# Performance work log

Measured on AMD Instinct MI355X. Metric: run time of the kernel, lower is better.

The kernel has to match this reference:

```python
import jax, jax.numpy as jnp
import numpy as np

B, T, DIM = 1, 2048, 4096
N_HEADS, N_KV_HEADS, HEAD_DIM = 32, 8, 128
N_REP = N_HEADS // N_KV_HEADS
ROPE_THETA = 10000.0


def setup_inputs() -> dict:
    key = jax.random.key(0)
    ks = jax.random.split(key, 6)
    # rotary angle tables: [T, head_dim//2]
    inv_freq = 1.0 / (ROPE_THETA ** (np.arange(0, HEAD_DIM, 2, dtype=np.float32) / HEAD_DIM))
    angles = np.arange(T, dtype=np.float32)[:, None] * inv_freq[None, :]
    scale = 0.02
    return {
        "x": jax.random.normal(ks[0], (B, T, DIM), dtype=jnp.float32),
        "rope_cos": jnp.asarray(np.cos(angles)),
        "rope_sin": jnp.asarray(np.sin(angles)),
        "wq": jax.random.normal(ks[1], (DIM, N_HEADS * HEAD_DIM), dtype=jnp.float32) * scale,
        "wk": jax.random.normal(ks[2], (DIM, N_KV_HEADS * HEAD_DIM), dtype=jnp.float32) * scale,
        "wv": jax.random.normal(ks[3], (DIM, N_KV_HEADS * HEAD_DIM), dtype=jnp.float32) * scale,
        "wo": jax.random.normal(ks[4], (N_HEADS * HEAD_DIM, DIM), dtype=jnp.float32) * scale,
    }


def _apply_rope(x, cos, sin):
    # x: [B, T, H, D]; cos/sin: [T, D//2] -- complex multiply on (even, odd) pairs
    xr = x.astype(jnp.float32).reshape(*x.shape[:-1], -1, 2)
    a, b = xr[..., 0], xr[..., 1]
    c = cos[None, : x.shape[1], None, :]
    s = sin[None, : x.shape[1], None, :]
    rot = jnp.stack([a * c - b * s, a * s + b * c], axis=-1)
    return rot.reshape(x.shape).astype(x.dtype)


def reference(x, rope_cos, rope_sin, wq, wk, wv, wo):
    Bq, Tq, _ = x.shape
    q = (x @ wq).reshape(Bq, Tq, N_HEADS, HEAD_DIM)
    k = (x @ wk).reshape(Bq, Tq, N_KV_HEADS, HEAD_DIM)
    v = (x @ wv).reshape(Bq, Tq, N_KV_HEADS, HEAD_DIM)
    q = _apply_rope(q, rope_cos, rope_sin)
    k = _apply_rope(k, rope_cos, rope_sin)
    # GQA: group query heads with their shared KV head instead of materializing repeated K/V
    qg = q.reshape(Bq, Tq, N_KV_HEADS, N_REP, HEAD_DIM)
    scale = 1.0 / jnp.sqrt(jnp.asarray(HEAD_DIM, dtype=q.dtype))
    scores = jnp.einsum("bqgrd,bkgd->bgrqk", qg, k) * scale  # [B,G,R,T,T]
    causal = jnp.tril(jnp.ones((Tq, Tq), dtype=bool))
    scores = jnp.where(causal[None, None, None], scores, jnp.finfo(scores.dtype).min)
    attn = jax.nn.softmax(scores, axis=-1)
    ctx = jnp.einsum("bgrqk,bkgd->bqgrd", attn, v).reshape(Bq, Tq, N_HEADS * HEAD_DIM)
    return ctx @ wo
```

## Files before the change

kernel.cpp:

```cpp
#include <hip/hip_runtime.h>
#include <hip/hip_bf16.h>

#define T_SEQ 2048
#define DIM 4096
#define NH 32
#define NKV 8
#define HD 128
#define QKV_N 6144

typedef __bf16 bf16x8 __attribute__((ext_vector_type(8)));
typedef float f32x4 __attribute__((ext_vector_type(4)));

__device__ __forceinline__ void storev(float* p, float v) { *p = v; }
__device__ __forceinline__ void storev(__hip_bfloat16* p, float v) { *p = __float2bfloat16(v); }

__device__ __forceinline__ float bf2f(unsigned short u) {
    unsigned int t = ((unsigned int)u) << 16;
    return __builtin_bit_cast(float, t);
}

__device__ __forceinline__ void gl_lds16(const __hip_bfloat16* g, __hip_bfloat16* l) {
    __builtin_amdgcn_global_load_lds(
        (const __attribute__((address_space(1))) unsigned int*)g,
        (__attribute__((address_space(3))) unsigned int*)l, 16, 0, 0);
}

__global__ void cast_x(const float* __restrict__ in, __hip_bfloat16* __restrict__ out, int n) {
    int i = (blockIdx.x * 256 + threadIdx.x) * 4;
    if (i < n) {
        float4 v = *(const float4*)(in + i);
        out[i + 0] = __float2bfloat16(v.x);
        out[i + 1] = __float2bfloat16(v.y);
        out[i + 2] = __float2bfloat16(v.z);
        out[i + 3] = __float2bfloat16(v.w);
    }
}

__global__ void tcast(const float* __restrict__ in, __hip_bfloat16* __restrict__ out,
                      int R, int C, int out_stride, int row_off) {
    __shared__ float tile[64][65];
    int tid = threadIdx.x;
    int r0 = blockIdx.y * 64, c0 = blockIdx.x * 64;
    for (int it = 0; it < 4; it++) {
        int row = (tid >> 4) + 16 * it;
        int c4 = (tid & 15) * 4;
        float4 v = *(const float4*)&in[(size_t)(r0 + row) * C + c0 + c4];
        tile[row][c4 + 0] = v.x;
        tile[row][c4 + 1] = v.y;
        tile[row][c4 + 2] = v.z;
        tile[row][c4 + 3] = v.w;
    }
    __syncthreads();
    for (int it = 0; it < 2; it++) {
        int orow = (tid >> 3) + 32 * it;
        int oc8 = (tid & 7) * 8;
        __hip_bfloat16 tmp[8];
        for (int j = 0; j < 8; j++)
            tmp[j] = __float2bfloat16(tile[oc8 + j][orow]);
        *(uint4*)&out[(size_t)(c0 + orow + row_off) * out_stride + r0 + oc8] = *(uint4*)tmp;
    }
}

__global__ void vtrans(const __hip_bfloat16* __restrict__ qkv, __hip_bfloat16* __restrict__ vt) {
    __shared__ __hip_bfloat16 tile[32][33];
    int tx = threadIdx.x, ty = threadIdx.y;
    int t0 = blockIdx.x * 32, d0 = blockIdx.y * 32, g = blockIdx.z;
    for (int k = 0; k < 4; k++)
        tile[ty + 8 * k][tx] = qkv[(size_t)(t0 + ty + 8 * k) * QKV_N + 5120 + g * HD + d0 + tx];
    __syncthreads();
    for (int k = 0; k < 4; k++)
        vt[(size_t)g * HD * T_SEQ + (size_t)(d0 + ty + 8 * k) * T_SEQ + t0 + tx] =
            tile[tx][ty + 8 * k];
}

__global__ void rope_kernel(__hip_bfloat16* qkv, const float* __restrict__ cosb,
                            const float* __restrict__ sinb) {
    int idx = blockIdx.x * 256 + threadIdx.x;
    int t = idx / 640;
    int col = (idx % 640) * 8;
    int i0 = (col & 127) >> 1;
    float f = col < DIM ? 0.08838834764831845f : 1.0f;
    size_t base = (size_t)t * QKV_N + col;
    unsigned short u[8];
    *(uint4*)u = *(const uint4*)&qkv[base];
    float4 cv = *(const float4*)&cosb[t * 64 + i0];
    float4 sv = *(const float4*)&sinb[t * 64 + i0];
    float c[4] = {cv.x, cv.y, cv.z, cv.w}, s[4] = {sv.x, sv.y, sv.z, sv.w};
    __hip_bfloat16 o[8];
    for (int j = 0; j < 4; j++) {
        float a = bf2f(u[2 * j]), b = bf2f(u[2 * j + 1]);
        o[2 * j]     = __float2bfloat16((a * c[j] - b * s[j]) * f);
        o[2 * j + 1] = __float2bfloat16((a * s[j] + b * c[j]) * f);
    }
    *(uint4*)&qkv[base] = *(uint4*)o;
}

template <typename OutT>
__global__ __launch_bounds__(256, 2) void gemm_bt(const __hip_bfloat16* __restrict__ A,
                                                  const __hip_bfloat16* __restrict__ Bt,
                                                  OutT* __restrict__ C, int M, int N, int K) {
    __shared__ __hip_bfloat16 sA[2][128 * 32];
    __shared__ __hip_bfloat16 sB[2][128 * 32];
    int tid = threadIdx.x;
    int wave = tid >> 6, lane = tid & 63, quad = lane >> 4, l15 = lane & 15;
    int wm = wave >> 1, wn = wave & 1;
    int m0 = blockIdx.y * 128, n0 = blockIdx.x * 128;
    f32x4 acc[4][4] = {};
    for (int k0 = 0; k0 < K; k0 += 64) {
        __syncthreads();
        for (int r = 0; r < 2; r++) {
            int seg = tid + 256 * r;
            int row = seg >> 2, col = (seg & 3) * 8;
            gl_lds16(&A[(size_t)(m0 + row) * K + k0 + col],       &sA[0][row * 32 + col]);
            gl_lds16(&A[(size_t)(m0 + row) * K + k0 + 32 + col],  &sA[1][row * 32 + col]);
            gl_lds16(&Bt[(size_t)(n0 + row) * K + k0 + col],      &sB[0][row * 32 + col]);
            gl_lds16(&Bt[(size_t)(n0 + row) * K + k0 + 32 + col], &sB[1][row * 32 + col]);
        }
        __syncthreads();
        for (int ks = 0; ks < 2; ks++) {
            bf16x8 af[4], bfr[4];
            for (int i = 0; i < 4; i++)
                af[i] = *(const bf16x8*)&sA[ks][(wm * 64 + i * 16 + l15) * 32 + quad * 8];
            for (int j = 0; j < 4; j++)
                bfr[j] = *(const bf16x8*)&sB[ks][(wn * 64 + j * 16 + l15) * 32 + quad * 8];
            for (int i = 0; i < 4; i++)
                for (int j = 0; j < 4; j++)
                    acc[i][j] = __builtin_amdgcn_mfma_f32_16x16x32_bf16(af[i], bfr[j], acc[i][j], 0, 0, 0);
        }
    }
    for (int i = 0; i < 4; i++)
        for (int j = 0; j < 4; j++)
            for (int r = 0; r < 4; r++) {
                int row = m0 + wm * 64 + i * 16 + quad * 4 + r;
                int col = n0 + wn * 64 + j * 16 + l15;
                storev(&C[(size_t)row * N + col], acc[i][j][r]);
            }
}

__global__ __launch_bounds__(256, 2) void attn_kernel(const __hip_bfloat16* __restrict__ qkv,
                                                      const __hip_bfloat16* __restrict__ vt,
                                                      __hip_bfloat16* __restrict__ ctx) {
    __shared__ __align__(16) __hip_bfloat16 sk[64][136];
    __shared__ __align__(16) __hip_bfloat16 sv[128][72];
    __shared__ __align__(16) __hip_bfloat16 sp[4][16][72];
    int tid = threadIdx.x;
    int wave = tid >> 6, lane = tid & 63, quad = lane >> 4, l15 = lane & 15;
    int pair = blockIdx.x, h = blockIdx.y, g = h >> 2;

    for (int rep = 0; rep < 2; rep++) {
        int qb = rep ? (31 - pair) : pair;
        int q0 = qb * 64 + wave * 16;

        bf16x8 qf[4];
        for (int ks = 0; ks < 4; ks++)
            qf[ks] = *(const bf16x8*)&qkv[(size_t)(q0 + l15) * QKV_N + h * HD + ks * 32 + quad * 8];

        f32x4 o[8] = {};
        float l_lane[4] = {0.f, 0.f, 0.f, 0.f};
        int nkt = qb + 1;

        for (int kt = 0; kt < nkt; kt++) {
            __syncthreads();
            for (int rr = 0; rr < 4; rr++) {
                int seg = tid + 256 * rr;
                {
                    int row = seg >> 4, col = (seg & 15) * 8;
                    *(uint4*)&sk[row][col] =
                        *(const uint4*)&qkv[(size_t)(kt * 64 + row) * QKV_N + DIM + g * HD + col];
                }
                {
                    int row = seg >> 3, col = (seg & 7) * 8;
                    *(uint4*)&sv[row][col] =
                        *(const uint4*)&vt[(size_t)g * HD * T_SEQ + (size_t)row * T_SEQ + kt * 64 + col];
                }
            }
            __syncthreads();
            f32x4 s[4] = {};
            for (int ks = 0; ks < 4; ks++)
                for (int n = 0; n < 4; n++) {
                    bf16x8 kf = *(const bf16x8*)&sk[n * 16 + l15][ks * 32 + quad * 8];
                    s[n] = __builtin_amdgcn_mfma_f32_16x16x32_bf16(qf[ks], kf, s[n], 0, 0, 0);
                }
            bool diag = (kt == qb);
            for (int r = 0; r < 4; r++) {
                float v0 = s[0][r], v1 = s[1][r], v2 = s[2][r], v3 = s[3][r];
                if (diag) {
                    int qrow = q0 + quad * 4 + r;
                    int k0i = kt * 64 + l15;
                    if (k0i      > qrow) v0 = -1e30f;
                    if (k0i + 16 > qrow) v1 = -1e30f;
                    if (k0i + 32 > qrow) v2 = -1e30f;
                    if (k0i + 48 > qrow) v3 = -1e30f;
                }
                float e0 = __expf(v0), e1 = __expf(v1);
                float e2 = __expf(v2), e3 = __expf(v3);
                l_lane[r] += (e0 + e1) + (e2 + e3);
                int qr = quad * 4 + r;
                sp[wave][qr][l15]      = __float2bfloat16(e0);
                sp[wave][qr][16 + l15] = __float2bfloat16(e1);
                sp[wave][qr][32 + l15] = __float2bfloat16(e2);
                sp[wave][qr][48 + l15] = __float2bfloat16(e3);
            }
            asm volatile("s_waitcnt lgkmcnt(0)" ::: "memory");
            bf16x8 pf0 = *(const bf16x8*)&sp[wave][l15][quad * 8];
            bf16x8 pf1 = *(const bf16x8*)&sp[wave][l15][32 + quad * 8];
            for (int j = 0; j < 8; j++) {
                bf16x8 vf0 = *(const bf16x8*)&sv[j * 16 + l15][quad * 8];
                bf16x8 vf1 = *(const bf16x8*)&sv[j * 16 + l15][32 + quad * 8];
                o[j] = __builtin_amdgcn_mfma_f32_16x16x32_bf16(pf0, vf0, o[j], 0, 0, 0);
                o[j] = __builtin_amdgcn_mfma_f32_16x16x32_bf16(pf1, vf1, o[j], 0, 0, 0);
            }
        }
        float rl[4];
        for (int r = 0; r < 4; r++) {
            float rs = l_lane[r];
            for (int off = 1; off < 16; off <<= 1) rs += __shfl_xor(rs, off);
            rl[r] = 1.f / rs;
        }
        for (int j = 0; j < 8; j++)
            for (int r = 0; r < 4; r++) {
                int row = q0 + quad * 4 + r;
                int col = h * HD + j * 16 + l15;
                ctx[(size_t)row * DIM + col] = __float2bfloat16(o[j][r] * rl[r]);
            }
    }
}

extern "C" void kernel_launch(void* const* d_in, const int* in_sizes, int n_in,
                              void* d_out, int out_size, void* d_ws, size_t ws_size,
                              hipStream_t stream) {
    const float* x        = (const float*)d_in[0];
    const float* rope_cos = (const float*)d_in[1];
    const float* rope_sin = (const float*)d_in[2];
    const float* wq       = (const float*)d_in[3];
    const float* wk       = (const float*)d_in[4];
    const float* wv       = (const float*)d_in[5];
    const float* wo       = (const float*)d_in[6];
    float* out = (float*)d_out;

    char* ws = (char*)d_ws;
    size_t need = 0;
    need += (size_t)T_SEQ * DIM * 2;
    need += (size_t)QKV_N * DIM * 2;
    need += (size_t)DIM * DIM * 2;
    need += (size_t)T_SEQ * QKV_N * 2;
    need += (size_t)NKV * HD * T_SEQ * 2;
    need += (size_t)T_SEQ * DIM * 2;
    if (ws_size < need) return;

    __hip_bfloat16* x_bf   = (__hip_bfloat16*)ws; ws += (size_t)T_SEQ * DIM * 2;
    __hip_bfloat16* wqkv_t = (__hip_bfloat16*)ws; ws += (size_t)QKV_N * DIM * 2;
    __hip_bfloat16* wo_t   = (__hip_bfloat16*)ws; ws += (size_t)DIM * DIM * 2;
    __hip_bfloat16* qkv    = (__hip_bfloat16*)ws; ws += (size_t)T_SEQ * QKV_N * 2;
    __hip_bfloat16* vt     = (__hip_bfloat16*)ws; ws += (size_t)NKV * HD * T_SEQ * 2;
    __hip_bfloat16* ctx    = (__hip_bfloat16*)ws; ws += (size_t)T_SEQ * DIM * 2;

    cast_x<<<8192, 256, 0, stream>>>(x, x_bf, T_SEQ * DIM);
    tcast<<<dim3(64, 64), 256, 0, stream>>>(wq, wqkv_t, DIM, 4096, 4096, 0);
    tcast<<<dim3(16, 64), 256, 0, stream>>>(wk, wqkv_t, DIM, 1024, 4096, 4096);
    tcast<<<dim3(16, 64), 256, 0, stream>>>(wv, wqkv_t, DIM, 1024, 4096, 5120);
    tcast<<<dim3(64, 64), 256, 0, stream>>>(wo, wo_t, DIM, 4096, 4096, 0);

    gemm_bt<__hip_bfloat16><<<dim3(48, 16), 256, 0, stream>>>(x_bf, wqkv_t, qkv, T_SEQ, QKV_N, DIM);
    rope_kernel<<<5120, 256, 0, stream>>>(qkv, rope_cos, rope_sin);
    vtrans<<<dim3(64, 4, 8), dim3(32, 8), 0, stream>>>(qkv, vt);
    attn_kernel<<<dim3(16, 32), 256, 0, stream>>>(qkv, vt, ctx);
    gemm_bt<float><<<dim3(32, 16), 256, 0, stream>>>(ctx, wo_t, out, T_SEQ, DIM, DIM);
}
```

Baseline: 491.0 us.

## Add 256x256 pipelined GEMM kernel for fused QKV projection

Adds a new 512-thread GEMM with 256x256 output tiles. It uses multi-stage direct global-to-LDS loads interleaved with MFMA phases, explicit barriers and waitcnts, raised wave priority during MFMA, and an XCD-aware block swizzle. It replaces the 128x128 gemm_bt for the QKV projection to get more data reuse per tile and to overlap memory with compute. The cost is fewer blocks (192 against 256 CUs) and heavy register use from the 8x4 accumulator tile per wave.

```diff
diff --git a/kernel.cpp b/kernel.cpp
--- a/kernel.cpp
+++ b/kernel.cpp
@@ -93,6 +93,105 @@
         o[2 * j + 1] = __float2bfloat16((a * s[j] + b * c[j]) * f);
     }
     *(uint4*)&qkv[base] = *(uint4*)o;
+}
+
+template <typename OutT>
+__global__ __launch_bounds__(512, 2) void gemm256(const __hip_bfloat16* __restrict__ A,
+                                                  const __hip_bfloat16* __restrict__ Bt,
+                                                  OutT* __restrict__ C, int N, int K) {
+    __shared__ __align__(16) __hip_bfloat16 sA[2][2][8192];
+    __shared__ __align__(16) __hip_bfloat16 sB[2][2][8192];
+    int tid = threadIdx.x;
+    int wave = tid >> 6, lane = tid & 63, quad = lane >> 4, l15 = lane & 15;
+    int wm = wave >> 2, wn = wave & 3;
+
+    int flat = blockIdx.x;
+    int nb = N >> 8;
+    int swz = ((gridDim.x & 7) == 0) ? ((flat & 7) * (gridDim.x >> 3) + (flat >> 3)) : flat;
+    int m0 = (swz / nb) << 8;
+    int n0 = (swz % nb) << 8;
+
+    const __hip_bfloat16* aThr = A  + (size_t)(m0 + l15) * K + (quad << 3);
+    const __hip_bfloat16* bThr = Bt + (size_t)(n0 + l15) * K + (quad << 3);
+    int NT = K >> 6;
+
+#define GSTAGE_A(BUF, KS, KCOL) do { \
+    gl_lds16(aThr + (size_t)(wave)     * 16 * K + (KCOL), &sA[BUF][KS][(wave) * 512]);     \
+    gl_lds16(aThr + (size_t)(wave + 8) * 16 * K + (KCOL), &sA[BUF][KS][(wave + 8) * 512]); \
+} while (0)
+#define GSTAGE_B(BUF, KS, KCOL) do { \
+    gl_lds16(bThr + (size_t)(wave)     * 16 * K + (KCOL), &sB[BUF][KS][(wave) * 512]);     \
+    gl_lds16(bThr + (size_t)(wave + 8) * 16 * K + (KCOL), &sB[BUF][KS][(wave + 8) * 512]); \
+} while (0)
+#define LDFA(BUF, KS, MH) do { _Pragma("unroll") \
+    for (int i_ = 0; i_ < 4; i_++) \
+        af[i_] = *(const bf16x8*)&sA[BUF][KS][(wm * 8 + (MH) * 4 + i_) * 512 + lane * 8]; } while (0)
+#define LDFB(BUF, KS) do { _Pragma("unroll") \
+    for (int j_ = 0; j_ < 4; j_++) \
+        bfr[j_] = *(const bf16x8*)&sB[BUF][KS][(wn * 4 + j_) * 512 + lane * 8]; } while (0)
+#define MFMA16(MH) do { _Pragma("unroll") \
+    for (int i_ = 0; i_ < 4; i_++) { _Pragma("unroll") \
+        for (int j_ = 0; j_ < 4; j_++) \
+            acc[(MH) * 4 + i_][j_] = __builtin_amdgcn_mfma_f32_16x16x32_bf16( \
+                af[i_], bfr[j_], acc[(MH) * 4 + i_][j_], 0, 0, 0); } } while (0)
+#define PHASE(BUF, KS, MH, LOADB, STAGE_STMT, CHK_STMT) do { \
+    bf16x8 af[4]; \
+    LDFA(BUF, KS, MH); \
+    if (LOADB) LDFB(BUF, KS); \
+    STAGE_STMT; \
+    CHK_STMT; \
+    __builtin_amdgcn_s_barrier(); \
+    asm volatile("s_waitcnt lgkmcnt(0)" ::: "memory"); \
+    __builtin_amdgcn_sched_barrier(0); \
+    __builtin_amdgcn_s_setprio(1); \
+    MFMA16(MH); \
+    __builtin_amdgcn_s_setprio(0); \
+    __builtin_amdgcn_s_barrier(); \
+} while (0)
+
+    f32x4 acc[8][4] = {};
+    bf16x8 bfr[4];
+
+    GSTAGE_A(0, 0, 0);
+    GSTAGE_B(0, 0, 0);
+    GSTAGE_A(0, 1, 32);
+    GSTAGE_B(0, 1, 32);
+    GSTAGE_A(1, 0, 64);
+    GSTAGE_B(1, 0, 64);
+    asm volatile("s_waitcnt vmcnt(4)" ::: "memory");
+    __builtin_amdgcn_s_barrier();
+
+    int niter = K >> 7;
+    for (int it = 0; it < niter; ++it) {
+        int t = it << 1;
+        int k1 = (t + 1) << 6;
+        int k2 = (t + 2 < NT ? t + 2 : 0) << 6;
+        int k3 = (t + 3 < NT ? t + 3 : 0) << 6;
+        PHASE(0, 0, 0, 1, GSTAGE_A(1, 1, k1 + 32), (void)0);
+        PHASE(0, 0, 1, 0, GSTAGE_B(1, 1, k1 + 32), (void)0);
+        PHASE(0, 1, 0, 1, GSTAGE_A(0, 0, k2),      (void)0);
+        PHASE(0, 1, 1, 0, GSTAGE_B(0, 0, k2),
+              asm volatile("s_waitcnt vmcnt(4)" ::: "memory"));
+        PHASE(1, 0, 0, 1, GSTAGE_A(0, 1, k2 + 32), (void)0);
+        PHASE(1, 0, 1, 0, GSTAGE_B(0, 1, k2 + 32), (void)0);
+        PHASE(1, 1, 0, 1, GSTAGE_A(1, 0, k3),      (void)0);
+        PHASE(1, 1, 1, 0, GSTAGE_B(1, 0, k3),
+              asm volatile("s_waitcnt vmcnt(4)" ::: "memory"));
+    }
+
+    for (int i = 0; i < 8; i++)
+        for (int j = 0; j < 4; j++)
+            for (int r = 0; r < 4; r++) {
+                int row = m0 + wm * 128 + i * 16 + quad * 4 + r;
+                int col = n0 + wn * 64 + j * 16 + l15;
+                storev(&C[(size_t)row * N + col], acc[i][j][r]);
+            }
+#undef GSTAGE_A
+#undef GSTAGE_B
+#undef LDFA
+#undef LDFB
+#undef MFMA16
+#undef PHASE
 }
 
 template <typename OutT>
@@ -261,7 +360,7 @@
     tcast<<<dim3(16, 64), 256, 0, stream>>>(wv, wqkv_t, DIM, 1024, 4096, 5120);
     tcast<<<dim3(64, 64), 256, 0, stream>>>(wo, wo_t, DIM, 4096, 4096, 0);
 
-    gemm_bt<__hip_bfloat16><<<dim3(48, 16), 256, 0, stream>>>(x_bf, wqkv_t, qkv, T_SEQ, QKV_N, DIM);
+    gemm256<__hip_bfloat16><<<192, 512, 0, stream>>>(x_bf, wqkv_t, qkv, QKV_N, DIM);
     rope_kernel<<<5120, 256, 0, stream>>>(qkv, rope_cos, rope_sin);
     vtrans<<<dim3(64, 4, 8), dim3(32, 8), 0, stream>>>(qkv, vt);
     attn_kernel<<<dim3(16, 32), 256, 0, stream>>>(qkv, vt, ctx);
```

Result: slower. 528.1 us (+7.6%).

## Double-buffer attention K/V tiles with direct global-to-LDS loads in MFMA fragment layout

Applied to the files above, without the earlier changes.

Replaces the synchronous register-staged copy of K and V tiles into shared memory with global_load_lds direct copies into two ping-pong buffers. The next tile is prefetched while the current tile's QK^T and PV MFMAs run. Tiles are stored pre-swizzled in MFMA fragment order, so each lane reads a contiguous 16 bytes. This is meant to hide global load latency and remove a barrier per iteration, at the cost of double the K/V LDS footprint, which could affect occupancy.

```diff
diff --git a/kernel.cpp b/kernel.cpp
--- a/kernel.cpp
+++ b/kernel.cpp
@@ -140,12 +140,30 @@
 __global__ __launch_bounds__(256, 2) void attn_kernel(const __hip_bfloat16* __restrict__ qkv,
                                                       const __hip_bfloat16* __restrict__ vt,
                                                       __hip_bfloat16* __restrict__ ctx) {
-    __shared__ __align__(16) __hip_bfloat16 sk[64][136];
-    __shared__ __align__(16) __hip_bfloat16 sv[128][72];
+    __shared__ __align__(16) __hip_bfloat16 skf[2][16][512];
+    __shared__ __align__(16) __hip_bfloat16 svf[2][16][512];
     __shared__ __align__(16) __hip_bfloat16 sp[4][16][72];
     int tid = threadIdx.x;
     int wave = tid >> 6, lane = tid & 63, quad = lane >> 4, l15 = lane & 15;
     int pair = blockIdx.x, h = blockIdx.y, g = h >> 2;
+    int q8 = quad * 8;
+
+    const __hip_bfloat16* kp[4];
+    const __hip_bfloat16* vp[4];
+    for (int i = 0; i < 4; i++) {
+        int s = wave * 4 + i;
+        kp[i] = qkv + (size_t)((s & 3) * 16 + l15) * QKV_N + DIM + g * HD + (s >> 2) * 32 + q8;
+        vp[i] = vt + (size_t)g * HD * T_SEQ + (size_t)((s >> 1) * 16 + l15) * T_SEQ + (s & 1) * 32 + q8;
+    }
+
+#define ATTN_STAGE(BUF, KT) do { \
+    _Pragma("unroll") \
+    for (int i_ = 0; i_ < 4; i_++) { \
+        int s_ = wave * 4 + i_; \
+        gl_lds16(kp[i_] + (size_t)(KT) * 64 * QKV_N, &skf[BUF][s_][0]); \
+        gl_lds16(vp[i_] + (KT) * 64,                 &svf[BUF][s_][0]); \
+    } \
+} while (0)
 
     for (int rep = 0; rep < 2; rep++) {
         int qb = rep ? (31 - pair) : pair;
@@ -159,26 +177,18 @@
         float l_lane[4] = {0.f, 0.f, 0.f, 0.f};
         int nkt = qb + 1;
 
+        ATTN_STAGE(0, 0);
+        asm volatile("s_waitcnt vmcnt(0)" ::: "memory");
+        __syncthreads();
+
         for (int kt = 0; kt < nkt; kt++) {
-            __syncthreads();
-            for (int rr = 0; rr < 4; rr++) {
-                int seg = tid + 256 * rr;
-                {
-                    int row = seg >> 4, col = (seg & 15) * 8;
-                    *(uint4*)&sk[row][col] =
-                        *(const uint4*)&qkv[(size_t)(kt * 64 + row) * QKV_N + DIM + g * HD + col];
-                }
-                {
-                    int row = seg >> 3, col = (seg & 7) * 8;
-                    *(uint4*)&sv[row][col] =
-                        *(const uint4*)&vt[(size_t)g * HD * T_SEQ + (size_t)row * T_SEQ + kt * 64 + col];
-                }
-            }
-            __syncthreads();
+            int cur = kt & 1;
+            if (kt + 1 < nkt) ATTN_STAGE(cur ^ 1, kt + 1);
+
             f32x4 s[4] = {};
             for (int ks = 0; ks < 4; ks++)
                 for (int n = 0; n < 4; n++) {
-                    bf16x8 kf = *(const bf16x8*)&sk[n * 16 + l15][ks * 32 + quad * 8];
+                    bf16x8 kf = *(const bf16x8*)&skf[cur][ks * 4 + n][lane * 8];
                     s[n] = __builtin_amdgcn_mfma_f32_16x16x32_bf16(qf[ks], kf, s[n], 0, 0, 0);
                 }
             bool diag = (kt == qb);
@@ -205,11 +215,13 @@
             bf16x8 pf0 = *(const bf16x8*)&sp[wave][l15][quad * 8];
             bf16x8 pf1 = *(const bf16x8*)&sp[wave][l15][32 + quad * 8];
             for (int j = 0; j < 8; j++) {
-                bf16x8 vf0 = *(const bf16x8*)&sv[j * 16 + l15][quad * 8];
-                bf16x8 vf1 = *(const bf16x8*)&sv[j * 16 + l15][32 + quad * 8];
+                bf16x8 vf0 = *(const bf16x8*)&svf[cur][j * 2 + 0][lane * 8];
+                bf16x8 vf1 = *(const bf16x8*)&svf[cur][j * 2 + 1][lane * 8];
                 o[j] = __builtin_amdgcn_mfma_f32_16x16x32_bf16(pf0, vf0, o[j], 0, 0, 0);
                 o[j] = __builtin_amdgcn_mfma_f32_16x16x32_bf16(pf1, vf1, o[j], 0, 0, 0);
             }
+            asm volatile("s_waitcnt vmcnt(0)" ::: "memory");
+            __syncthreads();
         }
         float rl[4];
         for (int r = 0; r < 4; r++) {
@@ -224,6 +236,7 @@
                 ctx[(size_t)row * DIM + col] = __float2bfloat16(o[j][r] * rl[r]);
             }
     }
+#undef ATTN_STAGE
 }
 
 extern "C" void kernel_launch(void* const* d_in, const int* in_sizes, int n_in,
```

After: 495.7 us. About the same (+1.0%).
